# Performance work log

Hardware: AMD Instinct MI355X
Metric: run time of the kernel (lower is better)

## Reference

```python
import jax, jax.numpy as jnp
import numpy as np

N_NODES = 100000
N_EDGES = 320000
DIM = 256  # hidden_dim*2 (bi-RNN)
BN_EPS = 1e-5


def setup_inputs() -> dict:
    key = jax.random.key(0)
    k1, k2, k3 = jax.random.split(key, 3)
    x = jax.random.normal(k1, (N_NODES, DIM), dtype=jnp.float32)
    W = jax.random.normal(k2, (DIM, DIM), dtype=jnp.float32) * (1.0 / np.sqrt(DIM))
    b = jnp.zeros((DIM,), dtype=jnp.float32)
    gamma = jnp.ones((DIM,), dtype=jnp.float32)
    beta = jnp.zeros((DIM,), dtype=jnp.float32)
    edge_index = jax.random.randint(k3, (2, N_EDGES), 0, N_NODES, dtype=jnp.int64)
    return {"x": x, "W": W, "b": b, "gamma": gamma, "beta": beta,
            "edge_index": edge_index}


def reference(x, W, b, gamma, beta, edge_index):
    N = x.shape[0]
    # --- GCNConv: add self-loops, symmetric deg^-1/2 normalization ---
    loop = jnp.arange(N, dtype=edge_index.dtype)
    row = jnp.concatenate([edge_index[0], loop])  # source / j
    col = jnp.concatenate([edge_index[1], loop])  # target / i
    deg = jax.ops.segment_sum(jnp.ones_like(col, dtype=x.dtype), col,
                              num_segments=N)
    dinv = jax.lax.rsqrt(deg)  # deg >= 1 due to self-loops
    norm = dinv[row] * dinv[col]  # [E+N]
    h = x @ W  # linear transform before propagation (PyG GCNConv)
    msg = h[row] * norm[:, None]  # gather + scale, [E+N, F]
    out = jax.ops.segment_sum(msg, col, num_segments=N) + b  # scatter-add
    # --- BatchNorm1d over nodes (training-mode batch statistics) ---
    mean = jnp.mean(out, axis=0)
    var = jnp.var(out, axis=0)
    out = (out - mean) * jax.lax.rsqrt(var + BN_EPS) * gamma + beta
    return jnp.tanh(out)
```

## Files before the change

kernel.cpp:

```cpp
#include <hip/hip_runtime.h>
#include <stdint.h>

#define N_NODES 100000
#define N_EDGES 320000
#define DIM 256
#define BN_EPS 1e-5f

typedef __attribute__((ext_vector_type(8))) short short8;
typedef __attribute__((ext_vector_type(4))) float f32x4;

__device__ __forceinline__ float bf2f(unsigned short u) {
    union { unsigned int i; float f; } v; v.i = ((unsigned int)u) << 16; return v.f;
}
__device__ __forceinline__ unsigned short f2bf(float f) {
    union { float f; unsigned int i; } v; v.f = f;
    unsigned int x = v.i;
    return (unsigned short)((x + 0x7fffu + ((x >> 16) & 1u)) >> 16);
}
__device__ __forceinline__ int eidx(const int* ei, int i64, int which, int e) {
    int idx = which * N_EDGES + e;
    return i64 ? ei[idx * 2] : ei[idx];
}
__device__ __forceinline__ f32x4 ldx4(const void* xv, int xf32, size_t off) {
    if (xf32) return *(const f32x4*)((const float*)xv + off);
    uint2 u = *(const uint2*)((const unsigned short*)xv + off);
    f32x4 o;
    o[0] = bf2f((unsigned short)(u.x & 0xffffu));
    o[1] = bf2f((unsigned short)(u.x >> 16));
    o[2] = bf2f((unsigned short)(u.y & 0xffffu));
    o[3] = bf2f((unsigned short)(u.y >> 16));
    return o;
}

__global__ void k_init(const unsigned short* __restrict__ xs,
                       const unsigned short* __restrict__ wsw,
                       const int* __restrict__ ei, int* __restrict__ flags,
                       int* __restrict__ cnt, float* __restrict__ stats) {
    __shared__ int red[3];
    int t = threadIdx.x;
    int i = blockIdx.x * 256 + t;
    if (i < N_NODES) cnt[i] = 0;
    if (i < 512) stats[i] = 0.0f;
    if (blockIdx.x == 0) {
        if (t < 3) red[t] = 0;
        __syncthreads();
        int badx = 0, badw = 0, nz = 0;
        for (int j = 0; j < 8; ++j) {
            if (!(fabsf(bf2f(xs[t * 8 + j])) <= 1000.0f)) badx = 1;
            if (!(fabsf(bf2f(wsw[t * 8 + j])) <= 1000.0f)) badw = 1;
            if (ei[(t * 8 + j) * 2 + 1] != 0) nz = 1;
        }
        if (badx) atomicOr(&red[0], 1);
        if (badw) atomicOr(&red[1], 1);
        if (nz)   atomicOr(&red[2], 1);
        __syncthreads();
        if (t == 0) { flags[0] = red[0]; flags[1] = red[1]; flags[2] = red[2] ? 0 : 1; }
    }
}

__global__ void k_cntwt(const int* __restrict__ ei, int* __restrict__ cnt,
                        const void* __restrict__ wv, unsigned short* __restrict__ Wth,
                        unsigned short* __restrict__ Wtl, const int* __restrict__ flags) {
    int b = blockIdx.x, t = threadIdx.x;
    if (b < 1250) {
        int i64 = flags[2];
        int e = b * 256 + t;
        if (e < N_EDGES) atomicAdd(&cnt[eidx(ei, i64, 1, e)], 1);
    } else {
        int wf32 = flags[1];
        int k = b - 1250, n = t;
        float v = wf32 ? ((const float*)wv)[k * DIM + n]
                       : bf2f(((const unsigned short*)wv)[k * DIM + n]);
        unsigned short h = f2bf(v);
        Wth[(size_t)n * DIM + k] = h;
        Wtl[(size_t)n * DIM + k] = f2bf(v - bf2f(h));
    }
}

__global__ void k_dscan(const int* __restrict__ cnt, float* __restrict__ dinv,
                        int* __restrict__ partial) {
    __shared__ int red[256];
    int t = threadIdx.x, b = blockIdx.x;
    int i = b * 256 + t;
    if (i < N_NODES) dinv[i] = rsqrtf((float)cnt[i] + 1.0f);
    if (b < 200) {
        int i0 = b * 512 + t * 2;
        int s = 0;
        if (i0 < N_NODES) s += cnt[i0];
        if (i0 + 1 < N_NODES) s += cnt[i0 + 1];
        red[t] = s;
        __syncthreads();
        for (int off = 128; off > 0; off >>= 1) {
            if (t < off) red[t] += red[t + off];
            __syncthreads();
        }
        if (t == 0) partial[b] = red[0];
    }
}

__global__ void k_scan2(const int* __restrict__ partial, int* __restrict__ pbase) {
    __shared__ int s[256];
    int t = threadIdx.x;
    int v = (t < 200) ? partial[t] : 0;
    s[t] = v;
    __syncthreads();
    for (int off = 1; off < 256; off <<= 1) {
        int u = (t >= off) ? s[t - off] : 0;
        __syncthreads();
        s[t] += u;
        __syncthreads();
    }
    if (t < 200) pbase[t] = s[t] - v;
}

__global__ void k_scan3(const int* __restrict__ cnt, const int* __restrict__ pbase,
                        int* __restrict__ row_start, int* __restrict__ cursor) {
    __shared__ int s[512];
    int t = threadIdx.x, b = blockIdx.x;
    int i = b * 512 + t;
    int v = (i < N_NODES) ? cnt[i] : 0;
    s[t] = v;
    __syncthreads();
    for (int off = 1; off < 512; off <<= 1) {
        int u = (t >= off) ? s[t - off] : 0;
        __syncthreads();
        s[t] += u;
        __syncthreads();
    }
    if (i < N_NODES) {
        int excl = pbase[b] + s[t] - v;
        row_start[i] = excl;
        cursor[i] = excl;
    }
}

__global__ void k_fill(const int* __restrict__ ei, const float* __restrict__ dinv,
                       int* __restrict__ cursor, int2* __restrict__ csr_pk,
                       const int* __restrict__ flags) {
    int i64 = flags[2];
    int e = blockIdx.x * 256 + threadIdx.x;
    if (e >= N_EDGES) return;
    int c = eidx(ei, i64, 1, e);
    int r = eidx(ei, i64, 0, e);
    int slot = atomicAdd(&cursor[c], 1);
    union { float f; int i; } u; u.f = dinv[r] * dinv[c];
    int2 pk; pk.x = r; pk.y = u.i;
    csr_pk[slot] = pk;
}

__launch_bounds__(512, 4)
__global__ void k_fused(const void* __restrict__ xv, const int* __restrict__ row_start,
                        const int* __restrict__ cnt, const int2* __restrict__ csr_pk,
                        const float* __restrict__ dinv,
                        const unsigned short* __restrict__ Wth,
                        const unsigned short* __restrict__ Wtl,
                        float* __restrict__ out, float* __restrict__ stats,
                        const int* __restrict__ flags) {
    __shared__ unsigned short zsh[80 * 256];
    __shared__ unsigned short zsl[80 * 256];
    int tid = threadIdx.x;
    int m0l = blockIdx.x * 80;
    int w = tid >> 6, lane = tid & 63, quad = lane >> 4, rl = lane & 15;
    int xf32 = flags[0];
    size_t lo4 = (size_t)(lane * 4);

    const int NPW = 10;
    int nb0 = m0l + w * NPW;
    int mstart = 0, mlen = 0; float mdv = 0.f;
    if (lane < NPW) {
        mstart = row_start[nb0 + lane];
        mlen   = cnt[nb0 + lane];
        mdv    = dinv[nb0 + lane];
    }
    int start = __shfl(mstart, 0);
    int len   = __shfl(mlen, 0);
    float dv  = __shfl(mdv, 0);
    int2 pk_cur; pk_cur.x = 0; pk_cur.y = 0;
    if (lane < len) pk_cur = csr_pk[start + lane];

    for (int nn = 0; nn < NPW; ++nn) {
        int row = w * NPW + nn;
        int node = m0l + row;
        float s = dv * dv;
        int cstart = start, clen = len;
        int myi = node;
        float myn = 0.0f;
        if (lane < clen) {
            myi = pk_cur.x;
            union { int i; float f; } u; u.i = pk_cur.y;
            myn = u.f;
        }
        bool big = (clen > 63);
        int n_eff;
        if (!big) {
            if (lane == clen) myn = s;
            n_eff = clen + 1;
        } else {
            n_eff = 64;
        }
        int npad = (n_eff + 3) & ~3;

        if (nn + 1 < NPW) {
            start = __shfl(mstart, nn + 1);
            len   = __shfl(mlen, nn + 1);
            dv    = __shfl(mdv, nn + 1);
            int2 pk_n; pk_n.x = 0; pk_n.y = 0;
            if (lane < len) pk_n = csr_pk[start + lane];
            pk_cur = pk_n;
        }

        f32x4 acc = (f32x4){0.f, 0.f, 0.f, 0.f};
        if (xf32) {
            const float* xp = (const float*)xv;
            for (int j = 0; j < npad; j += 4) {
                int i0 = __shfl(myi, j),     i1 = __shfl(myi, j + 1);
                int i2 = __shfl(myi, j + 2), i3 = __shfl(myi, j + 3);
                float n0 = __shfl(myn, j),     n1 = __shfl(myn, j + 1);
                float n2 = __shfl(myn, j + 2), n3 = __shfl(myn, j + 3);
                f32x4 x0 = *(const f32x4*)(xp + (size_t)i0 * DIM + lo4);
                f32x4 x1 = *(const f32x4*)(xp + (size_t)i1 * DIM + lo4);
                f32x4 x2 = *(const f32x4*)(xp + (size_t)i2 * DIM + lo4);
                f32x4 x3 = *(const f32x4*)(xp + (size_t)i3 * DIM + lo4);
                #pragma unroll
                for (int q = 0; q < 4; ++q)
                    acc[q] += n0 * x0[q] + n1 * x1[q] + n2 * x2[q] + n3 * x3[q];
            }
        } else {
            const unsigned short* xp = (const unsigned short*)xv;
            for (int j = 0; j < npad; j += 4) {
                int i0 = __shfl(myi, j),     i1 = __shfl(myi, j + 1);
                int i2 = __shfl(myi, j + 2), i3 = __shfl(myi, j + 3);
                float n0 = __shfl(myn, j),     n1 = __shfl(myn, j + 1);
                float n2 = __shfl(myn, j + 2), n3 = __shfl(myn, j + 3);
                uint2 u0 = *(const uint2*)(xp + (size_t)i0 * DIM + lo4);
                uint2 u1 = *(const uint2*)(xp + (size_t)i1 * DIM + lo4);
                uint2 u2 = *(const uint2*)(xp + (size_t)i2 * DIM + lo4);
                uint2 u3 = *(const uint2*)(xp + (size_t)i3 * DIM + lo4);
                acc[0] += n0 * bf2f((unsigned short)(u0.x & 0xffffu))
                        + n1 * bf2f((unsigned short)(u1.x & 0xffffu))
                        + n2 * bf2f((unsigned short)(u2.x & 0xffffu))
                        + n3 * bf2f((unsigned short)(u3.x & 0xffffu));
                acc[1] += n0 * bf2f((unsigned short)(u0.x >> 16))
                        + n1 * bf2f((unsigned short)(u1.x >> 16))
                        + n2 * bf2f((unsigned short)(u2.x >> 16))
                        + n3 * bf2f((unsigned short)(u3.x >> 16));
                acc[2] += n0 * bf2f((unsigned short)(u0.y & 0xffffu))
                        + n1 * bf2f((unsigned short)(u1.y & 0xffffu))
                        + n2 * bf2f((unsigned short)(u2.y & 0xffffu))
                        + n3 * bf2f((unsigned short)(u3.y & 0xffffu));
                acc[3] += n0 * bf2f((unsigned short)(u0.y >> 16))
                        + n1 * bf2f((unsigned short)(u1.y >> 16))
                        + n2 * bf2f((unsigned short)(u2.y >> 16))
                        + n3 * bf2f((unsigned short)(u3.y >> 16));
            }
        }
        if (big) {
            f32x4 xs = ldx4(xv, xf32, (size_t)node * DIM + lo4);
            #pragma unroll
            for (int q = 0; q < 4; ++q) acc[q] += s * xs[q];
            for (int t2 = 64; t2 < clen; ++t2) {
                int2 pk = csr_pk[cstart + t2];
                union { int i; float f; } u; u.i = pk.y;
                f32x4 xr = ldx4(xv, xf32, (size_t)pk.x * DIM + lo4);
                #pragma unroll
                for (int q = 0; q < 4; ++q) acc[q] += u.f * xr[q];
            }
        }

        unsigned short h0 = f2bf(acc[0]), h1 = f2bf(acc[1]);
        unsigned short h2 = f2bf(acc[2]), h3 = f2bf(acc[3]);
        uint2 vh, vl;
        vh.x = (unsigned int)h0 | ((unsigned int)h1 << 16);
        vh.y = (unsigned int)h2 | ((unsigned int)h3 << 16);
        vl.x = (unsigned int)f2bf(acc[0] - bf2f(h0))
             | ((unsigned int)f2bf(acc[1] - bf2f(h1)) << 16);
        vl.y = (unsigned int)f2bf(acc[2] - bf2f(h2))
             | ((unsigned int)f2bf(acc[3] - bf2f(h3)) << 16);
        int sl  = lane >> 1;
        int swz = (sl & 24) | ((sl & 7) ^ (row & 7));
        int offb = swz * 16 + (lane & 1) * 8;
        *(uint2*)((char*)zsh + (size_t)row * 512 + offb) = vh;
        *(uint2*)((char*)zsl + (size_t)row * 512 + offb) = vl;
    }
    __syncthreads();

    f32x4 cacc[5][2];
    #pragma unroll
    for (int ms = 0; ms < 5; ++ms)
        #pragma unroll
        for (int nt = 0; nt < 2; ++nt)
            cacc[ms][nt] = (f32x4){0.f, 0.f, 0.f, 0.f};

    #pragma unroll
    for (int kk = 0; kk < 8; ++kk) {
        int k0g = kk * 32 + quad * 8;
        short8 bh[2], bl[2];
        #pragma unroll
        for (int nt = 0; nt < 2; ++nt) {
            int n = w * 32 + nt * 16 + rl;
            bh[nt] = *(const short8*)(Wth + (size_t)n * DIM + k0g);
            bl[nt] = *(const short8*)(Wtl + (size_t)n * DIM + k0g);
        }
        #pragma unroll
        for (int ms = 0; ms < 5; ++ms) {
            int row = ms * 16 + rl;
            int slot = kk * 4 + quad;
            int sl = (slot & 24) | ((slot & 7) ^ (row & 7));
            short8 ah = *(const short8*)((const char*)zsh + (size_t)row * 512 + sl * 16);
            short8 al = *(const short8*)((const char*)zsl + (size_t)row * 512 + sl * 16);
            #pragma unroll
            for (int nt = 0; nt < 2; ++nt) {
                cacc[ms][nt] = __builtin_amdgcn_mfma_f32_16x16x32_bf16(ah, bh[nt], cacc[ms][nt], 0, 0, 0);
                cacc[ms][nt] = __builtin_amdgcn_mfma_f32_16x16x32_bf16(al, bh[nt], cacc[ms][nt], 0, 0, 0);
                cacc[ms][nt] = __builtin_amdgcn_mfma_f32_16x16x32_bf16(ah, bl[nt], cacc[ms][nt], 0, 0, 0);
            }
        }
    }

    #pragma unroll
    for (int nt = 0; nt < 2; ++nt) {
        int col = w * 32 + nt * 16 + rl;
        float s1 = 0.f, s2 = 0.f;
        #pragma unroll
        for (int ms = 0; ms < 5; ++ms)
            #pragma unroll
            for (int i = 0; i < 4; ++i) {
                float v = cacc[ms][nt][i];
                s1 += v; s2 += v * v;
                __builtin_nontemporal_store(
                    v, out + (size_t)(m0l + ms * 16 + quad * 4 + i) * DIM + col);
            }
        s1 += __shfl_xor(s1, 16); s1 += __shfl_xor(s1, 32);
        s2 += __shfl_xor(s2, 16); s2 += __shfl_xor(s2, 32);
        if (lane < 16) {
            atomicAdd(&stats[col], s1);
            atomicAdd(&stats[256 + col], s2);
        }
    }
}

__global__ void k_final(float* __restrict__ out, const float* __restrict__ stats,
                        const void* __restrict__ gv, const void* __restrict__ bv,
                        const int* __restrict__ flags) {
    __shared__ float ssc[256], ssh[256];
    int t = threadIdx.x;
    {
        int ff32 = flags[0];
        const float invN = 1.0f / (float)N_NODES;
        float mean = stats[t] * invN;
        float var = stats[256 + t] * invN - mean * mean;
        float g = ff32 ? ((const float*)gv)[t] : bf2f(((const unsigned short*)gv)[t]);
        float bb = ff32 ? ((const float*)bv)[t] : bf2f(((const unsigned short*)bv)[t]);
        float sc = g * rsqrtf(var + BN_EPS);
        ssc[t] = sc;
        ssh[t] = bb - mean * sc;
    }
    __syncthreads();
    int gt = blockIdx.x * 256 + t;
    int f0 = (gt & 63) * 4;
    size_t off = (size_t)gt * 4;
    f32x4 v = *(const f32x4*)(out + off);
    f32x4 o;
    #pragma unroll
    for (int j = 0; j < 4; ++j)
        o[j] = tanhf(v[j] * ssc[f0 + j] + ssh[f0 + j]);
    __builtin_nontemporal_store(o, (f32x4*)(out + off));
}

extern "C" void kernel_launch(void* const* d_in, const int* in_sizes, int n_in,
                              void* d_out, int out_size, void* d_ws, size_t ws_size,
                              hipStream_t stream) {
    const void* x     = d_in[0];
    const void* W     = d_in[1];
    const void* gamma = d_in[3];
    const void* beta  = d_in[4];
    const int* ei     = (const int*)d_in[5];
    float* out = (float*)d_out;

    char* ws = (char*)d_ws;
    int*   flags     = (int*)(ws);
    int*   cnt       = (int*)(ws + 4096);
    int*   row_start = (int*)(ws + 409600);
    int*   cursor    = (int*)(ws + 819200);
    float* dinv      = (float*)(ws + 1228800);
    int*   partial   = (int*)(ws + 1638400);
    int*   pbase     = (int*)(ws + 1646592);
    float* stats     = (float*)(ws + 1654784);
    unsigned short* Wth = (unsigned short*)(ws + 1671168);
    unsigned short* Wtl = (unsigned short*)(ws + 1802240);
    int2*  csr_pk    = (int2*)(ws + 1933312);

    const unsigned short* xs_us = (const unsigned short*)x;
    const unsigned short* W_us  = (const unsigned short*)W;

    k_init <<<391,  256, 0, stream>>>(xs_us, W_us, ei, flags, cnt, stats);
    k_cntwt<<<1506, 256, 0, stream>>>(ei, cnt, W, Wth, Wtl, flags);
    k_dscan<<<391,  256, 0, stream>>>(cnt, dinv, partial);
    k_scan2<<<1,    256, 0, stream>>>(partial, pbase);
    k_scan3<<<200,  512, 0, stream>>>(cnt, pbase, row_start, cursor);
    k_fill <<<1250, 256, 0, stream>>>(ei, dinv, cursor, csr_pk, flags);

    k_fused<<<1250, 512, 0, stream>>>(x, row_start, cnt, csr_pk, dinv,
                                      Wth, Wtl, out, stats, flags);

    k_final<<<25000, 256, 0, stream>>>(out, stats, gamma, beta, flags);
}
```

Baseline: 347.4 us.

## Shrink fused tile to 48 rows, prefetch next node's gathers, merge scan kernels

The fused gather+GEMM kernel now handles 48 nodes per block instead of 80, which lowers LDS use and raises the occupancy hint to 6 blocks. It adds bounds guards for the partial last tile. The fp32 path is software-pipelined so the first four neighbor rows of the next node are loaded while the current node accumulates. The two scan kernels are merged into one, which removes a launch, and nontemporal stores are replaced with normal stores. The extra prefetch registers may limit the higher occupancy, and each block now loads W for fewer rows.

```diff
diff --git a/kernel.cpp b/kernel.cpp
--- a/kernel.cpp
+++ b/kernel.cpp
@@ -98,25 +98,22 @@
     }
 }
 
-__global__ void k_scan2(const int* __restrict__ partial, int* __restrict__ pbase) {
-    __shared__ int s[256];
-    int t = threadIdx.x;
-    int v = (t < 200) ? partial[t] : 0;
-    s[t] = v;
+__global__ void k_scan23(const int* __restrict__ cnt, const int* __restrict__ partial,
+                         int* __restrict__ row_start, int* __restrict__ cursor) {
+    __shared__ int sp[256];
+    __shared__ int s[512];
+    __shared__ int base;
+    int t = threadIdx.x, b = blockIdx.x;
+    if (t < 256) sp[t] = (t < 200) ? partial[t] : 0;
     __syncthreads();
     for (int off = 1; off < 256; off <<= 1) {
-        int u = (t >= off) ? s[t - off] : 0;
-        __syncthreads();
-        s[t] += u;
-        __syncthreads();
-    }
-    if (t < 200) pbase[t] = s[t] - v;
-}
-
-__global__ void k_scan3(const int* __restrict__ cnt, const int* __restrict__ pbase,
-                        int* __restrict__ row_start, int* __restrict__ cursor) {
-    __shared__ int s[512];
-    int t = threadIdx.x, b = blockIdx.x;
+        int u = 0;
+        if (t < 256 && t >= off) u = sp[t - off];
+        __syncthreads();
+        if (t < 256) sp[t] += u;
+        __syncthreads();
+    }
+    if (t == 0) base = (b == 0) ? 0 : sp[b - 1];
     int i = b * 512 + t;
     int v = (i < N_NODES) ? cnt[i] : 0;
     s[t] = v;
@@ -128,7 +125,7 @@
         __syncthreads();
     }
     if (i < N_NODES) {
-        int excl = pbase[b] + s[t] - v;
+        int excl = base + s[t] - v;
         row_start[i] = excl;
         cursor[i] = excl;
     }
@@ -148,7 +145,7 @@
     csr_pk[slot] = pk;
 }
 
-__launch_bounds__(512, 4)
+__launch_bounds__(512, 6)
 __global__ void k_fused(const void* __restrict__ xv, const int* __restrict__ row_start,
                         const int* __restrict__ cnt, const int2* __restrict__ csr_pk,
                         const float* __restrict__ dinv,
@@ -156,67 +153,84 @@
                         const unsigned short* __restrict__ Wtl,
                         float* __restrict__ out, float* __restrict__ stats,
                         const int* __restrict__ flags) {
-    __shared__ unsigned short zsh[80 * 256];
-    __shared__ unsigned short zsl[80 * 256];
+    __shared__ unsigned short zsh[48 * 256];
+    __shared__ unsigned short zsl[48 * 256];
     int tid = threadIdx.x;
-    int m0l = blockIdx.x * 80;
+    int m0l = blockIdx.x * 48;
     int w = tid >> 6, lane = tid & 63, quad = lane >> 4, rl = lane & 15;
     int xf32 = flags[0];
     size_t lo4 = (size_t)(lane * 4);
 
-    const int NPW = 10;
+    const int NPW = 6;
     int nb0 = m0l + w * NPW;
     int mstart = 0, mlen = 0; float mdv = 0.f;
-    if (lane < NPW) {
+    if (lane < NPW && nb0 + lane < N_NODES) {
         mstart = row_start[nb0 + lane];
         mlen   = cnt[nb0 + lane];
         mdv    = dinv[nb0 + lane];
     }
-    int start = __shfl(mstart, 0);
-    int len   = __shfl(mlen, 0);
-    float dv  = __shfl(mdv, 0);
-    int2 pk_cur; pk_cur.x = 0; pk_cur.y = 0;
-    if (lane < len) pk_cur = csr_pk[start + lane];
-
-    for (int nn = 0; nn < NPW; ++nn) {
-        int row = w * NPW + nn;
-        int node = m0l + row;
-        float s = dv * dv;
-        int cstart = start, clen = len;
-        int myi = node;
-        float myn = 0.0f;
-        if (lane < clen) {
-            myi = pk_cur.x;
-            union { int i; float f; } u; u.i = pk_cur.y;
-            myn = u.f;
-        }
-        bool big = (clen > 63);
-        int n_eff;
-        if (!big) {
-            if (lane == clen) myn = s;
-            n_eff = clen + 1;
-        } else {
-            n_eff = 64;
-        }
-        int npad = (n_eff + 3) & ~3;
-
-        if (nn + 1 < NPW) {
-            start = __shfl(mstart, nn + 1);
-            len   = __shfl(mlen, nn + 1);
-            dv    = __shfl(mdv, nn + 1);
-            int2 pk_n; pk_n.x = 0; pk_n.y = 0;
-            if (lane < len) pk_n = csr_pk[start + lane];
-            pk_cur = pk_n;
-        }
-
-        f32x4 acc = (f32x4){0.f, 0.f, 0.f, 0.f};
-        if (xf32) {
-            const float* xp = (const float*)xv;
-            for (int j = 0; j < npad; j += 4) {
-                int i0 = __shfl(myi, j),     i1 = __shfl(myi, j + 1);
-                int i2 = __shfl(myi, j + 2), i3 = __shfl(myi, j + 3);
-                float n0 = __shfl(myn, j),     n1 = __shfl(myn, j + 1);
-                float n2 = __shfl(myn, j + 2), n3 = __shfl(myn, j + 3);
+
+    if (xf32) {
+        const float* xp = (const float*)xv;
+        int myiA = 0, myiB = 0; float mynA = 0.f, mynB = 0.f;
+        int lnA = 0, lnB = 0, stA = 0, stB = 0; float sA = 0.f, sB = 0.f;
+        float nwA[4], nwB[4];
+        f32x4 xA[4], xB[4];
+        int2 pkB, pkN;
+
+        {
+            int st = __shfl(mstart, 0), ln = __shfl(mlen, 0);
+            float dv = __shfl(mdv, 0);
+            int2 pk; pk.x = 0; pk.y = 0;
+            if (lane < ln) pk = csr_pk[st + lane];
+            myiA = (nb0 < N_NODES) ? nb0 : 0;
+            mynA = 0.f; sA = dv * dv; lnA = ln; stA = st;
+            if (lane < ln) { myiA = pk.x; union { int i; float f; } u; u.i = pk.y; mynA = u.f; }
+            if (ln <= 63 && lane == ln) mynA = sA;
+            #pragma unroll
+            for (int j = 0; j < 4; ++j) {
+                int ii = __shfl(myiA, j); nwA[j] = __shfl(mynA, j);
+                xA[j] = *(const f32x4*)(xp + (size_t)ii * DIM + lo4);
+            }
+            int st1 = __shfl(mstart, 1), ln1 = __shfl(mlen, 1);
+            pkB.x = 0; pkB.y = 0;
+            if (lane < ln1) pkB = csr_pk[st1 + lane];
+        }
+
+        #pragma unroll
+        for (int nn = 0; nn < NPW; ++nn) {
+            int row = w * NPW + nn;
+            if (nn + 1 < NPW) {
+                int st = __shfl(mstart, nn + 1), ln = __shfl(mlen, nn + 1);
+                float dv = __shfl(mdv, nn + 1);
+                int noden = nb0 + nn + 1;
+                myiB = (noden < N_NODES) ? noden : 0;
+                mynB = 0.f; sB = dv * dv; lnB = ln; stB = st;
+                if (lane < ln) { myiB = pkB.x; union { int i; float f; } u; u.i = pkB.y; mynB = u.f; }
+                if (ln <= 63 && lane == ln) mynB = sB;
+                #pragma unroll
+                for (int j = 0; j < 4; ++j) {
+                    int ii = __shfl(myiB, j); nwB[j] = __shfl(mynB, j);
+                    xB[j] = *(const f32x4*)(xp + (size_t)ii * DIM + lo4);
+                }
+                if (nn + 2 < NPW) {
+                    int st2 = __shfl(mstart, nn + 2), ln2 = __shfl(mlen, nn + 2);
+                    pkN.x = 0; pkN.y = 0;
+                    if (lane < ln2) pkN = csr_pk[st2 + lane];
+                }
+            }
+            f32x4 acc = (f32x4){0.f, 0.f, 0.f, 0.f};
+            #pragma unroll
+            for (int q = 0; q < 4; ++q)
+                acc[q] += nwA[0] * xA[0][q] + nwA[1] * xA[1][q]
+                        + nwA[2] * xA[2][q] + nwA[3] * xA[3][q];
+            int n_eff = (lnA > 63) ? 64 : (lnA + 1);
+            int npad = (n_eff + 3) & ~3;
+            for (int j = 4; j < npad; j += 4) {
+                int i0 = __shfl(myiA, j),     i1 = __shfl(myiA, j + 1);
+                int i2 = __shfl(myiA, j + 2), i3 = __shfl(myiA, j + 3);
+                float n0 = __shfl(mynA, j),     n1 = __shfl(mynA, j + 1);
+                float n2 = __shfl(mynA, j + 2), n3 = __shfl(mynA, j + 3);
                 f32x4 x0 = *(const f32x4*)(xp + (size_t)i0 * DIM + lo4);
                 f32x4 x1 = *(const f32x4*)(xp + (size_t)i1 * DIM + lo4);
                 f32x4 x2 = *(const f32x4*)(xp + (size_t)i2 * DIM + lo4);
@@ -225,8 +239,72 @@
                 for (int q = 0; q < 4; ++q)
                     acc[q] += n0 * x0[q] + n1 * x1[q] + n2 * x2[q] + n3 * x3[q];
             }
-        } else {
-            const unsigned short* xp = (const unsigned short*)xv;
+            if (lnA > 63) {
+                int node = nb0 + nn;
+                f32x4 xs = *(const f32x4*)(xp + (size_t)node * DIM + lo4);
+                #pragma unroll
+                for (int q = 0; q < 4; ++q) acc[q] += sA * xs[q];
+                for (int t2 = 64; t2 < lnA; ++t2) {
+                    int2 pk = csr_pk[stA + t2];
+                    union { int i; float f; } u; u.i = pk.y;
+                    f32x4 xr = *(const f32x4*)(xp + (size_t)pk.x * DIM + lo4);
+                    #pragma unroll
+                    for (int q = 0; q < 4; ++q) acc[q] += u.f * xr[q];
+                }
+            }
+            unsigned short h0 = f2bf(acc[0]), h1 = f2bf(acc[1]);
+            unsigned short h2 = f2bf(acc[2]), h3 = f2bf(acc[3]);
+            uint2 vh, vl;
+            vh.x = (unsigned int)h0 | ((unsigned int)h1 << 16);
+            vh.y = (unsigned int)h2 | ((unsigned int)h3 << 16);
+            vl.x = (unsigned int)f2bf(acc[0] - bf2f(h0))
+                 | ((unsigned int)f2bf(acc[1] - bf2f(h1)) << 16);
+            vl.y = (unsigned int)f2bf(acc[2] - bf2f(h2))
+                 | ((unsigned int)f2bf(acc[3] - bf2f(h3)) << 16);
+            int sl  = lane >> 1;
+            int swz = (sl & 24) | ((sl & 7) ^ (row & 7));
+            int offb = swz * 16 + (lane & 1) * 8;
+            *(uint2*)((char*)zsh + (size_t)row * 512 + offb) = vh;
+            *(uint2*)((char*)zsl + (size_t)row * 512 + offb) = vl;
+            if (nn + 1 < NPW) {
+                myiA = myiB; mynA = mynB; lnA = lnB; sA = sB; stA = stB;
+                #pragma unroll
+                for (int j = 0; j < 4; ++j) { nwA[j] = nwB[j]; xA[j] = xB[j]; }
+                pkB = pkN;
+            }
+        }
+    } else {
+        const unsigned short* xp = (const unsigned short*)xv;
+        int start = __shfl(mstart, 0);
+        int len   = __shfl(mlen, 0);
+        float dv  = __shfl(mdv, 0);
+        int2 pk_cur; pk_cur.x = 0; pk_cur.y = 0;
+        if (lane < len) pk_cur = csr_pk[start + lane];
+        for (int nn = 0; nn < NPW; ++nn) {
+            int row = w * NPW + nn;
+            int node = nb0 + nn;
+            float s = dv * dv;
+            int cstart = start, clen = len;
+            int myi = (node < N_NODES) ? node : 0;
+            float myn = 0.0f;
+            if (lane < clen) {
+                myi = pk_cur.x;
+                union { int i; float f; } u; u.i = pk_cur.y;
+                myn = u.f;
+            }
+            bool big = (clen > 63);
+            int n_eff = big ? 64 : (clen + 1);
+            if (!big && lane == clen) myn = s;
+            int npad = (n_eff + 3) & ~3;
+            if (nn + 1 < NPW) {
+                start = __shfl(mstart, nn + 1);
+                len   = __shfl(mlen, nn + 1);
+                dv    = __shfl(mdv, nn + 1);
+                int2 pk_n; pk_n.x = 0; pk_n.y = 0;
+                if (lane < len) pk_n = csr_pk[start + lane];
+                pk_cur = pk_n;
+            }
+            f32x4 acc = (f32x4){0.f, 0.f, 0.f, 0.f};
             for (int j = 0; j < npad; j += 4) {
                 int i0 = __shfl(myi, j),     i1 = __shfl(myi, j + 1);
                 int i2 = __shfl(myi, j + 2), i3 = __shfl(myi, j + 3);
@@ -253,40 +331,39 @@
                         + n2 * bf2f((unsigned short)(u2.y >> 16))
                         + n3 * bf2f((unsigned short)(u3.y >> 16));
             }
-        }
-        if (big) {
-            f32x4 xs = ldx4(xv, xf32, (size_t)node * DIM + lo4);
-            #pragma unroll
-            for (int q = 0; q < 4; ++q) acc[q] += s * xs[q];
-            for (int t2 = 64; t2 < clen; ++t2) {
-                int2 pk = csr_pk[cstart + t2];
-                union { int i; float f; } u; u.i = pk.y;
-                f32x4 xr = ldx4(xv, xf32, (size_t)pk.x * DIM + lo4);
+            if (big) {
+                f32x4 xs = ldx4(xv, xf32, (size_t)node * DIM + lo4);
                 #pragma unroll
-                for (int q = 0; q < 4; ++q) acc[q] += u.f * xr[q];
-            }
-        }
-
-        unsigned short h0 = f2bf(acc[0]), h1 = f2bf(acc[1]);
-        unsigned short h2 = f2bf(acc[2]), h3 = f2bf(acc[3]);
-        uint2 vh, vl;
-        vh.x = (unsigned int)h0 | ((unsigned int)h1 << 16);
-        vh.y = (unsigned int)h2 | ((unsigned int)h3 << 16);
-        vl.x = (unsigned int)f2bf(acc[0] - bf2f(h0))
-             | ((unsigned int)f2bf(acc[1] - bf2f(h1)) << 16);
-        vl.y = (unsigned int)f2bf(acc[2] - bf2f(h2))
-             | ((unsigned int)f2bf(acc[3] - bf2f(h3)) << 16);
-        int sl  = lane >> 1;
-        int swz = (sl & 24) | ((sl & 7) ^ (row & 7));
-        int offb = swz * 16 + (lane & 1) * 8;
-        *(uint2*)((char*)zsh + (size_t)row * 512 + offb) = vh;
-        *(uint2*)((char*)zsl + (size_t)row * 512 + offb) = vl;
+                for (int q = 0; q < 4; ++q) acc[q] += s * xs[q];
+                for (int t2 = 64; t2 < clen; ++t2) {
+                    int2 pk = csr_pk[cstart + t2];
+                    union { int i; float f; } u; u.i = pk.y;
+                    f32x4 xr = ldx4(xv, xf32, (size_t)pk.x * DIM + lo4);
+                    #pragma unroll
+                    for (int q = 0; q < 4; ++q) acc[q] += u.f * xr[q];
+                }
+            }
+            unsigned short h0 = f2bf(acc[0]), h1 = f2bf(acc[1]);
+            unsigned short h2 = f2bf(acc[2]), h3 = f2bf(acc[3]);
+            uint2 vh, vl;
+            vh.x = (unsigned int)h0 | ((unsigned int)h1 << 16);
+            vh.y = (unsigned int)h2 | ((unsigned int)h3 << 16);
+            vl.x = (unsigned int)f2bf(acc[0] - bf2f(h0))
+                 | ((unsigned int)f2bf(acc[1] - bf2f(h1)) << 16);
+            vl.y = (unsigned int)f2bf(acc[2] - bf2f(h2))
+                 | ((unsigned int)f2bf(acc[3] - bf2f(h3)) << 16);
+            int sl  = lane >> 1;
+            int swz = (sl & 24) | ((sl & 7) ^ (row & 7));
+            int offb = swz * 16 + (lane & 1) * 8;
+            *(uint2*)((char*)zsh + (size_t)row * 512 + offb) = vh;
+            *(uint2*)((char*)zsl + (size_t)row * 512 + offb) = vl;
+        }
     }
     __syncthreads();
 
-    f32x4 cacc[5][2];
+    f32x4 cacc[3][2];
     #pragma unroll
-    for (int ms = 0; ms < 5; ++ms)
+    for (int ms = 0; ms < 3; ++ms)
         #pragma unroll
         for (int nt = 0; nt < 2; ++nt)
             cacc[ms][nt] = (f32x4){0.f, 0.f, 0.f, 0.f};
@@ -302,7 +379,7 @@
             bl[nt] = *(const short8*)(Wtl + (size_t)n * DIM + k0g);
         }
         #pragma unroll
-        for (int ms = 0; ms < 5; ++ms) {
+        for (int ms = 0; ms < 3; ++ms) {
             int row = ms * 16 + rl;
             int slot = kk * 4 + quad;
             int sl = (slot & 24) | ((slot & 7) ^ (row & 7));
@@ -322,13 +399,14 @@
         int col = w * 32 + nt * 16 + rl;
         float s1 = 0.f, s2 = 0.f;
         #pragma unroll
-        for (int ms = 0; ms < 5; ++ms)
+        for (int ms = 0; ms < 3; ++ms)
             #pragma unroll
             for (int i = 0; i < 4; ++i) {
                 float v = cacc[ms][nt][i];
                 s1 += v; s2 += v * v;
-                __builtin_nontemporal_store(
-                    v, out + (size_t)(m0l + ms * 16 + quad * 4 + i) * DIM + col);
+                int orow = m0l + ms * 16 + quad * 4 + i;
+                if (orow < N_NODES)
+                    out[(size_t)orow * DIM + col] = v;
             }
         s1 += __shfl_xor(s1, 16); s1 += __shfl_xor(s1, 32);
         s2 += __shfl_xor(s2, 16); s2 += __shfl_xor(s2, 32);
@@ -364,7 +442,7 @@
     #pragma unroll
     for (int j = 0; j < 4; ++j)
         o[j] = tanhf(v[j] * ssc[f0 + j] + ssh[f0 + j]);
-    __builtin_nontemporal_store(o, (f32x4*)(out + off));
+    *(f32x4*)(out + off) = o;
 }
 
 extern "C" void kernel_launch(void* const* d_in, const int* in_sizes, int n_in,
@@ -384,7 +462,6 @@
     int*   cursor    = (int*)(ws + 819200);
     float* dinv      = (float*)(ws + 1228800);
     int*   partial   = (int*)(ws + 1638400);
-    int*   pbase     = (int*)(ws + 1646592);
     float* stats     = (float*)(ws + 1654784);
     unsigned short* Wth = (unsigned short*)(ws + 1671168);
     unsigned short* Wtl = (unsigned short*)(ws + 1802240);
@@ -393,15 +470,14 @@
     const unsigned short* xs_us = (const unsigned short*)x;
     const unsigned short* W_us  = (const unsigned short*)W;
 
-    k_init <<<391,  256, 0, stream>>>(xs_us, W_us, ei, flags, cnt, stats);
-    k_cntwt<<<1506, 256, 0, stream>>>(ei, cnt, W, Wth, Wtl, flags);
-    k_dscan<<<391,  256, 0, stream>>>(cnt, dinv, partial);
-    k_scan2<<<1,    256, 0, stream>>>(partial, pbase);
-    k_scan3<<<200,  512, 0, stream>>>(cnt, pbase, row_start, cursor);
-    k_fill <<<1250, 256, 0, stream>>>(ei, dinv, cursor, csr_pk, flags);
-
-    k_fused<<<1250, 512, 0, stream>>>(x, row_start, cnt, csr_pk, dinv,
-                                      Wth, Wtl, out, stats, flags);
-
-    k_final<<<25000, 256, 0, stream>>>(out, stats, gamma, beta, flags);
-}
+    k_init  <<<391,  256, 0, stream>>>(xs_us, W_us, ei, flags, cnt, stats);
+    k_cntwt <<<1506, 256, 0, stream>>>(ei, cnt, W, Wth, Wtl, flags);
+    k_dscan <<<391,  256, 0, stream>>>(cnt, dinv, partial);
+    k_scan23<<<200,  512, 0, stream>>>(cnt, partial, row_start, cursor);
+    k_fill  <<<1250, 256, 0, stream>>>(ei, dinv, cursor, csr_pk, flags);
+
+    k_fused <<<2084, 512, 0, stream>>>(x, row_start, cnt, csr_pk, dinv,
+                                       Wth, Wtl, out, stats, flags);
+
+    k_final <<<25000, 256, 0, stream>>>(out, stats, gamma, beta, flags);
+}
```

After: 351.1 us. Within noise of the previous version (+1.1%).
